# Optimization experiments

Hardware: AMD Instinct MI355X
Metric: run time of the kernel (lower is better)

The kernel has to match this reference:

```python
import jax, jax.numpy as jnp
import numpy as np

B, S, H, D = 4, 2048, 8, 64  # batch, seq, heads, per-head dim (dim=64)
EPS = 1e-5


def _layernorm(h, g, b):
    m = jnp.mean(h, axis=-1, keepdims=True)
    v = jnp.mean(jnp.square(h - m), axis=-1, keepdims=True)
    return (h - m) * jax.lax.rsqrt(v + EPS) * g + b


def setup_inputs() -> dict:
    key = jax.random.key(0)
    ks = jax.random.split(key, 12)
    s = 1.0 / np.sqrt(D)
    return {
        "x": jax.random.normal(ks[0], (B, S, H, D), dtype=jnp.float32),
        "ln1_g": jnp.ones((D,), jnp.float32),
        "ln1_b": jnp.zeros((D,), jnp.float32),
        "Wp": jax.random.normal(ks[1], (D, 3 * D), jnp.float32) * s,
        "bp": jnp.zeros((3 * D,), jnp.float32),
        "ln2_g": jnp.ones((D,), jnp.float32),
        "ln2_b": jnp.zeros((D,), jnp.float32),
        "W1": jax.random.normal(ks[2], (D, 4 * D), jnp.float32) * s,
        "b1": jnp.zeros((4 * D,), jnp.float32),
        "W2": jax.random.normal(ks[3], (4 * D, D), jnp.float32) * (1.0 / np.sqrt(4 * D)),
        "b2": jnp.zeros((D,), jnp.float32),
    }


def reference(x, ln1_g, ln1_b, Wp, bp, ln2_g, ln2_b, W1, b1, W2, b2):
    # x: [B, S, H, D]
    h = _layernorm(x, ln1_g, ln1_b)
    qkv = h @ Wp + bp                       # [B,S,H,3D]  (dropout = identity, eval)
    q, k, v = jnp.split(qkv, 3, axis=-1)
    q = q.transpose(0, 2, 1, 3)             # [B,H,S,D]
    k = k.transpose(0, 2, 1, 3)
    v = v.transpose(0, 2, 1, 3)
    sim = jnp.einsum('bhqd,bhkd->bhqk', q, k)   # no sqrt(d) scaling (faithful)
    attn = jax.nn.softmax(sim, axis=-1)
    out = jnp.einsum('bhqk,bhkd->bhqd', attn, v).transpose(0, 2, 1, 3)  # [B,S,H,D]
    out = _layernorm(out, ln2_g, ln2_b)
    out = jax.nn.gelu(out @ W1 + b1, approximate=False) @ W2 + b2
    return out + x
```

## Files before the change

kernel.cpp:

```cpp
#include <hip/hip_runtime.h>
#include <hip/hip_bf16.h>
#include <math.h>

#define BB 4
#define SS 2048
#define HH 8
#define DD 64
#define EPSV 1e-5f

typedef __attribute__((ext_vector_type(8))) short short8;
typedef __attribute__((ext_vector_type(4))) float f32x4;
typedef __attribute__((ext_vector_type(4))) unsigned int uint4v;
typedef unsigned short ushort_t;
#define MFMA16 __builtin_amdgcn_mfma_f32_16x16x32_bf16

__device__ inline unsigned short f2bf(float f) {
    unsigned u = __builtin_bit_cast(unsigned, f);
    unsigned r = (u + 0x7fffu + ((u >> 16) & 1u)) >> 16;
    return (unsigned short)r;
}
__device__ inline float bf2f(unsigned short h) {
    unsigned u = ((unsigned)h) << 16;
    return __builtin_bit_cast(float, u);
}
__device__ inline unsigned pkbf(float a, float b) {
    __hip_bfloat162 h2 = __float22bfloat162_rn(make_float2(a, b));
    unsigned u;
    __builtin_memcpy(&u, &h2, 4);
    return u;
}
__device__ inline float gelu_f(float v) {
    float a = v * 0.70710678118654752f;
    float z = fabsf(a);
    float t = __builtin_amdgcn_rcpf(fmaf(0.3275911f, z, 1.0f));
    float p = t * fmaf(t, fmaf(t, fmaf(t, fmaf(t, 1.061405429f, -1.453152027f),
                                       1.421413741f), -0.284496736f), 0.254829592f);
    float e = __builtin_amdgcn_exp2f(-z * z * 1.4426950408889634f);
    float erfz = fmaf(-p, e, 1.0f);
    float se = (a < 0.0f) ? -erfz : erfz;
    return 0.5f * v * (1.0f + se);
}

__global__ __launch_bounds__(256, 2) void k1_ln_qkv(
    const float* __restrict__ x, const float* __restrict__ g1, const float* __restrict__ b1v,
    const float* __restrict__ Wp, const float* __restrict__ bp,
    float* __restrict__ qws, ushort_t* __restrict__ khws, ushort_t* __restrict__ vtws)
{
    __shared__ __align__(16) ushort_t Hh[64 * 72];
    __shared__ __align__(16) ushort_t Hl[64 * 72];
    __shared__ __align__(16) ushort_t Vt[64 * 72];
    __shared__ __align__(16) ushort_t PadK1[13824];

    const int tid = threadIdx.x;
    const int wv  = tid >> 6;
    const int lane = tid & 63;
    const int l15 = lane & 15;
    const int g   = lane >> 4;
    const int bh  = blockIdx.x & 31;
    const int sc  = blockIdx.x >> 5;
    const int b   = bh >> 3, hh = bh & 7;
    const int s0  = sc * 64;

    PadK1[tid] = (ushort_t)tid;
    if (blockIdx.x == 0xFFFFFFFFu) {
        qws[tid] = (float)PadK1[255 - tid];
        return;
    }

    short8 bqh[2], bql[2], bkh[2], bkl[2], bvh[2];
    {
        const int nq = wv * 16 + l15;
        #pragma unroll
        for (int kh = 0; kh < 2; ++kh) {
            const int koff = kh * 32 + g * 8;
            #pragma unroll
            for (int j = 0; j < 8; ++j) {
                const float* wrow = Wp + (size_t)(koff + j) * 192 + nq;
                float wq = wrow[0];
                ushort_t hq = f2bf(wq);
                bqh[kh][j] = (short)hq;
                bql[kh][j] = (short)f2bf(wq - bf2f(hq));
                float wk = wrow[64];
                ushort_t hk = f2bf(wk);
                bkh[kh][j] = (short)hk;
                bkl[kh][j] = (short)f2bf(wk - bf2f(hk));
                bvh[kh][j] = (short)f2bf(wrow[128]);
            }
        }
    }
    const float biasq = bp[wv * 16 + l15];
    const float biask = bp[64 + wv * 16 + l15];
    const float biasv = bp[128 + wv * 16 + l15];

    {
        const int srow = s0 + wv * 16 + l15;
        const float* xr = x + ((size_t)(b * 2048 + srow) * 8 + hh) * 64;
        float hvv[16];
        #pragma unroll
        for (int kh = 0; kh < 2; ++kh) {
            float4 p0 = *(const float4*)(xr + kh * 32 + g * 8);
            float4 p1 = *(const float4*)(xr + kh * 32 + g * 8 + 4);
            hvv[kh*8+0]=p0.x; hvv[kh*8+1]=p0.y; hvv[kh*8+2]=p0.z; hvv[kh*8+3]=p0.w;
            hvv[kh*8+4]=p1.x; hvv[kh*8+5]=p1.y; hvv[kh*8+6]=p1.z; hvv[kh*8+7]=p1.w;
        }
        float s1 = 0.0f;
        #pragma unroll
        for (int i = 0; i < 16; ++i) s1 += hvv[i];
        s1 += __shfl_xor(s1, 16, 64);
        s1 += __shfl_xor(s1, 32, 64);
        float mean = s1 * (1.0f / 64.0f);
        float s2 = 0.0f;
        #pragma unroll
        for (int i = 0; i < 16; ++i) { float d = hvv[i] - mean; s2 += d * d; }
        s2 += __shfl_xor(s2, 16, 64);
        s2 += __shfl_xor(s2, 32, 64);
        float rstd = rsqrtf(s2 * (1.0f / 64.0f) + EPSV);

        #pragma unroll
        for (int kh = 0; kh < 2; ++kh) {
            ushort_t hi[8]; unsigned lo2[4];
            float hf[8];
            #pragma unroll
            for (int j = 0; j < 8; ++j) {
                int dI = kh * 32 + g * 8 + j;
                hf[j] = (hvv[kh*8+j] - mean) * rstd * g1[dI] + b1v[dI];
                hi[j] = f2bf(hf[j]);
            }
            uint4 HHv;
            HHv.x = (unsigned)hi[0] | ((unsigned)hi[1] << 16);
            HHv.y = (unsigned)hi[2] | ((unsigned)hi[3] << 16);
            HHv.z = (unsigned)hi[4] | ((unsigned)hi[5] << 16);
            HHv.w = (unsigned)hi[6] | ((unsigned)hi[7] << 16);
            #pragma unroll
            for (int j = 0; j < 4; ++j)
                lo2[j] = pkbf(hf[2*j] - bf2f(hi[2*j]), hf[2*j+1] - bf2f(hi[2*j+1]));
            uint4 HLv; HLv.x = lo2[0]; HLv.y = lo2[1]; HLv.z = lo2[2]; HLv.w = lo2[3];
            int off = (wv * 16 + l15) * 72 + kh * 32 + g * 8;
            *(uint4*)(&Hh[off]) = HHv;
            *(uint4*)(&Hl[off]) = HLv;
        }
    }
    __syncthreads();

    #pragma unroll
    for (int mt = 0; mt < 4; ++mt) {
        short8 ah[2], al[2];
        int abase = (mt * 16 + l15) * 72 + g * 8;
        ah[0] = *(const short8*)(&Hh[abase]);
        ah[1] = *(const short8*)(&Hh[abase + 32]);
        al[0] = *(const short8*)(&Hl[abase]);
        al[1] = *(const short8*)(&Hl[abase + 32]);

        f32x4 aq = (f32x4){0.f,0.f,0.f,0.f};
        f32x4 ak = (f32x4){0.f,0.f,0.f,0.f};
        f32x4 av = (f32x4){0.f,0.f,0.f,0.f};
        #pragma unroll
        for (int kh = 0; kh < 2; ++kh) {
            aq = MFMA16(ah[kh], bqh[kh], aq, 0, 0, 0);
            aq = MFMA16(al[kh], bqh[kh], aq, 0, 0, 0);
            aq = MFMA16(ah[kh], bql[kh], aq, 0, 0, 0);
            ak = MFMA16(ah[kh], bkh[kh], ak, 0, 0, 0);
            ak = MFMA16(al[kh], bkh[kh], ak, 0, 0, 0);
            ak = MFMA16(ah[kh], bkl[kh], ak, 0, 0, 0);
            av = MFMA16(ah[kh], bvh[kh], av, 0, 0, 0);
        }

        size_t base = ((size_t)bh * 2048 + s0 + mt * 16 + 4 * g) * 64 + wv * 16 + l15;
        #pragma unroll
        for (int r = 0; r < 4; ++r) {
            qws[base + (size_t)r * 64] = aq[r] + biasq;
            khws[base + (size_t)r * 64] = f2bf(ak[r] + biask);
        }
        uint2 vvp;
        vvp.x = pkbf(av[0] + biasv, av[1] + biasv);
        vvp.y = pkbf(av[2] + biasv, av[3] + biasv);
        *(uint2*)(&Vt[(wv * 16 + l15) * 72 + mt * 16 + 4 * g]) = vvp;
    }
    __syncthreads();

    #pragma unroll
    for (int p = 0; p < 2; ++p) {
        int slot = tid + 256 * p;
        int dd = slot >> 3, cc = slot & 7;
        int c0 = ((cc >> 2) << 5) + ((cc & 3) << 2);
        uint2 a = *(const uint2*)(&Vt[dd * 72 + c0]);
        uint2 b2 = *(const uint2*)(&Vt[dd * 72 + c0 + 16]);
        uint4 o; o.x = a.x; o.y = a.y; o.z = b2.x; o.w = b2.y;
        *(uint4*)(vtws + ((size_t)bh * 64 + dd) * 2048 + s0 + cc * 8) = o;
    }
}

#define NKT 32

__global__ __launch_bounds__(256, 2) void k2_attn(
    const float* __restrict__ qws, const ushort_t* __restrict__ khws,
    const ushort_t* __restrict__ vtws, float* __restrict__ ows)
{
    __shared__ __align__(16) ushort_t KhL[2][64 * 64];
    __shared__ __align__(16) ushort_t VtL[2][64 * 64];
    __shared__ __align__(16) ushort_t PadL[11264];

    const int tid  = threadIdx.x;
    const int w    = tid >> 6;
    const int lane = tid & 63;
    const int l15  = lane & 15;
    const int g    = lane >> 4;
    const int bh   = blockIdx.x & 31;
    const int qb0  = (blockIdx.x >> 5) * 128;

    PadL[tid] = (ushort_t)tid;
    if (blockIdx.x == 0xFFFFFFFFu) {
        ows[tid] = (float)PadL[255 - tid];
        return;
    }

    const float LOG2E = 1.4426950408889634f;
    short8 qh[2][2], ql[2][2];
    #pragma unroll
    for (int sub = 0; sub < 2; ++sub) {
        const float* qp = qws + ((size_t)bh * SS + qb0 + w * 32 + sub * 16 + l15) * 64;
        #pragma unroll
        for (int kh = 0; kh < 2; ++kh) {
            const float* p = qp + 32 * kh + 8 * g;
            #pragma unroll
            for (int j = 0; j < 8; ++j) {
                float f = p[j] * LOG2E;
                ushort_t hi = f2bf(f);
                qh[sub][kh][j] = (short)hi;
                ql[sub][kh][j] = (short)f2bf(f - bf2f(hi));
            }
        }
    }

    float lrow[2] = {0.0f, 0.0f};
    f32x4 oacc[2][4];
    #pragma unroll
    for (int sub = 0; sub < 2; ++sub)
        #pragma unroll
        for (int dt = 0; dt < 4; ++dt) oacc[sub][dt] = (f32x4){0.f, 0.f, 0.f, 0.f};

    const size_t kbase = (size_t)bh * SS * 64;
    const size_t vbase = (size_t)bh * 64 * 2048;

    const int dlo  = lane >> 3;
    const int j8   = ((lane & 7) ^ dlo) << 3;
    const int row0 = w * 8 + dlo;
    const int row1 = 32 + row0;
    const int lb0  = (64 * w) * 8;
    const int lb1  = (256 + 64 * w) * 8;

    #define K2_STAGE(buf, tg)                                                   \
        do {                                                                     \
            __builtin_amdgcn_global_load_lds(                                    \
                (const __attribute__((address_space(1))) void*)                  \
                    (khws + kbase + (size_t)((tg) * 64 + row0) * 64 + j8),       \
                (__attribute__((address_space(3))) void*)(&KhL[(buf)][lb0]),     \
                16, 0, 0);                                                       \
            __builtin_amdgcn_global_load_lds(                                    \
                (const __attribute__((address_space(1))) void*)                  \
                    (khws + kbase + (size_t)((tg) * 64 + row1) * 64 + j8),       \
                (__attribute__((address_space(3))) void*)(&KhL[(buf)][lb1]),     \
                16, 0, 0);                                                       \
            __builtin_amdgcn_global_load_lds(                                    \
                (const __attribute__((address_space(1))) void*)                  \
                    (vtws + vbase + (size_t)row0 * 2048 + (tg) * 64 + j8),       \
                (__attribute__((address_space(3))) void*)(&VtL[(buf)][lb0]),     \
                16, 0, 0);                                                       \
            __builtin_amdgcn_global_load_lds(                                    \
                (const __attribute__((address_space(1))) void*)                  \
                    (vtws + vbase + (size_t)row1 * 2048 + (tg) * 64 + j8),       \
                (__attribute__((address_space(3))) void*)(&VtL[(buf)][lb1]),     \
                16, 0, 0);                                                       \
        } while (0)

    K2_STAGE(0, 0);

    const int rsw = l15 & 7;

    for (int kt = 0; kt < NKT; ++kt) {
        __syncthreads();
        const int cur = kt & 1;

        if (kt < NKT - 1) K2_STAGE(cur ^ 1, kt + 1);

        #pragma unroll
        for (int half = 0; half < 2; ++half) {
            uint2 pA[2], pB[2];
            #pragma unroll
            for (int nf2 = 0; nf2 < 2; ++nf2) {
                const int nf = half * 2 + nf2;
                f32x4 aA = (f32x4){0.f, 0.f, 0.f, 0.f};
                f32x4 aB = (f32x4){0.f, 0.f, 0.f, 0.f};
                #pragma unroll
                for (int kh = 0; kh < 2; ++kh) {
                    short8 kah = *(const short8*)(
                        &KhL[cur][(nf * 16 + l15) * 64 + (((4 * kh + g) ^ rsw) << 3)]);
                    aA = MFMA16(kah, qh[0][kh], aA, 0, 0, 0);
                    aA = MFMA16(kah, ql[0][kh], aA, 0, 0, 0);
                    aB = MFMA16(kah, qh[1][kh], aB, 0, 0, 0);
                    aB = MFMA16(kah, ql[1][kh], aB, 0, 0, 0);
                }
                {
                    float p0 = __builtin_amdgcn_exp2f(aA[0]);
                    float p1 = __builtin_amdgcn_exp2f(aA[1]);
                    float p2 = __builtin_amdgcn_exp2f(aA[2]);
                    float p3 = __builtin_amdgcn_exp2f(aA[3]);
                    lrow[0] += (p0 + p1) + (p2 + p3);
                    pA[nf2].x = pkbf(p0, p1); pA[nf2].y = pkbf(p2, p3);
                }
                {
                    float p0 = __builtin_amdgcn_exp2f(aB[0]);
                    float p1 = __builtin_amdgcn_exp2f(aB[1]);
                    float p2 = __builtin_amdgcn_exp2f(aB[2]);
                    float p3 = __builtin_amdgcn_exp2f(aB[3]);
                    lrow[1] += (p0 + p1) + (p2 + p3);
                    pB[nf2].x = pkbf(p0, p1); pB[nf2].y = pkbf(p2, p3);
                }
            }
            short8 paA = __builtin_bit_cast(short8, (uint4v){pA[0].x, pA[0].y, pA[1].x, pA[1].y});
            short8 paB = __builtin_bit_cast(short8, (uint4v){pB[0].x, pB[0].y, pB[1].x, pB[1].y});
            #pragma unroll
            for (int dt = 0; dt < 4; ++dt) {
                short8 vbf = *(const short8*)(
                    &VtL[cur][(16 * dt + l15) * 64 + (((4 * half + g) ^ rsw) << 3)]);
                oacc[0][dt] = MFMA16(paA, vbf, oacc[0][dt], 0, 0, 0);
                oacc[1][dt] = MFMA16(paB, vbf, oacc[1][dt], 0, 0, 0);
            }
        }
    }

    #pragma unroll
    for (int sub = 0; sub < 2; ++sub) {
        float l = lrow[sub];
        l += __shfl_xor(l, 16, 64);
        l += __shfl_xor(l, 32, 64);
        float il = 1.0f / l;
        #pragma unroll
        for (int r = 0; r < 4; ++r) {
            float ilr = __shfl(il, 4 * g + r, 64);
            int row = qb0 + w * 32 + sub * 16 + 4 * g + r;
            #pragma unroll
            for (int dt = 0; dt < 4; ++dt)
                ows[((size_t)bh * SS + row) * 64 + dt * 16 + l15] = oacc[sub][dt][r] * ilr;
        }
    }
    #undef K2_STAGE
}

__global__ __launch_bounds__(256, 2) void k3_ln_mlp(
    const float* __restrict__ ows, const float* __restrict__ x,
    const float* __restrict__ g2, const float* __restrict__ b2v,
    const float* __restrict__ W1, const float* __restrict__ b1m,
    const float* __restrict__ W2, const float* __restrict__ b2o,
    float* __restrict__ out)
{
    __shared__ __align__(16) ushort_t Hb[64 * 72];
    __shared__ __align__(16) ushort_t Hs[16 * 264];
    __shared__ __align__(16) float Rs[4 * 16 * 72];
    __shared__ __align__(16) ushort_t PadK3[9600];

    const int tid  = threadIdx.x;
    const int wv   = tid >> 6;
    const int lane = tid & 63;
    const int l15  = lane & 15;
    const int g    = lane >> 4;

    PadK3[tid] = (ushort_t)tid;
    if (blockIdx.x == 0xFFFFFFFFu) {
        out[tid] = (float)PadK3[255 - tid];
        return;
    }

    short8 w1f[4][2], w2f[4][2];
    float  b1r[4][4];
    #pragma unroll
    for (int t = 0; t < 4; ++t) {
        #pragma unroll
        for (int kh = 0; kh < 2; ++kh) {
            #pragma unroll
            for (int j = 0; j < 8; ++j) {
                w1f[t][kh][j] = (short)f2bf(
                    W1[(size_t)(kh * 32 + g * 8 + j) * 256 + wv * 64 + t * 16 + l15]);
                w2f[t][kh][j] = (short)f2bf(
                    W2[(size_t)(wv * 64 + kh * 32 + g * 8 + j) * 64 + t * 16 + l15]);
            }
        }
        #pragma unroll
        for (int r = 0; r < 4; ++r)
            b1r[t][r] = b1m[wv * 64 + t * 16 + 4 * g + r];
    }

    const int r0 = blockIdx.x * 64;

    {
        const float* orow = ows + (size_t)(r0 + wv * 16 + l15) * 64;
        float hvv[16];
        #pragma unroll
        for (int kh = 0; kh < 2; ++kh) {
            float4 p0 = *(const float4*)(orow + kh * 32 + g * 8);
            float4 p1 = *(const float4*)(orow + kh * 32 + g * 8 + 4);
            hvv[kh*8+0]=p0.x; hvv[kh*8+1]=p0.y; hvv[kh*8+2]=p0.z; hvv[kh*8+3]=p0.w;
            hvv[kh*8+4]=p1.x; hvv[kh*8+5]=p1.y; hvv[kh*8+6]=p1.z; hvv[kh*8+7]=p1.w;
        }
        float s1 = 0.0f;
        #pragma unroll
        for (int i = 0; i < 16; ++i) s1 += hvv[i];
        s1 += __shfl_xor(s1, 16, 64);
        s1 += __shfl_xor(s1, 32, 64);
        float mean = s1 * (1.0f / 64.0f);
        float s2 = 0.0f;
        #pragma unroll
        for (int i = 0; i < 16; ++i) { float d = hvv[i] - mean; s2 += d * d; }
        s2 += __shfl_xor(s2, 16, 64);
        s2 += __shfl_xor(s2, 32, 64);
        float rstd = rsqrtf(s2 * (1.0f / 64.0f) + EPSV);

        #pragma unroll
        for (int kh = 0; kh < 2; ++kh) {
            ushort_t hi[8];
            #pragma unroll
            for (int j = 0; j < 8; ++j) {
                int dI = kh * 32 + g * 8 + j;
                hi[j] = f2bf((hvv[kh*8+j] - mean) * rstd * g2[dI] + b2v[dI]);
            }
            uint4 HHv;
            HHv.x = (unsigned)hi[0] | ((unsigned)hi[1] << 16);
            HHv.y = (unsigned)hi[2] | ((unsigned)hi[3] << 16);
            HHv.z = (unsigned)hi[4] | ((unsigned)hi[5] << 16);
            HHv.w = (unsigned)hi[6] | ((unsigned)hi[7] << 16);
            *(uint4*)(&Hb[(wv * 16 + l15) * 72 + kh * 32 + g * 8]) = HHv;
        }
    }
    __syncthreads();

    for (int mt = 0; mt < 4; ++mt) {
        short8 h2f[2];
        h2f[0] = *(const short8*)(&Hb[(mt * 16 + l15) * 72 + g * 8]);
        h2f[1] = *(const short8*)(&Hb[(mt * 16 + l15) * 72 + 32 + g * 8]);

        #pragma unroll
        for (int t = 0; t < 4; ++t) {
            f32x4 acc = (f32x4){0.f, 0.f, 0.f, 0.f};
            acc = MFMA16(w1f[t][0], h2f[0], acc, 0, 0, 0);
            acc = MFMA16(w1f[t][1], h2f[1], acc, 0, 0, 0);
            float ge[4];
            #pragma unroll
            for (int r = 0; r < 4; ++r)
                ge[r] = gelu_f(acc[r] + b1r[t][r]);
            uint2 pk;
            pk.x = pkbf(ge[0], ge[1]);
            pk.y = pkbf(ge[2], ge[3]);
            *(uint2*)(&Hs[l15 * 264 + wv * 64 + t * 16 + 4 * g]) = pk;
        }

        short8 ha[2];
        ha[0] = *(const short8*)(&Hs[l15 * 264 + wv * 64 + g * 8]);
        ha[1] = *(const short8*)(&Hs[l15 * 264 + wv * 64 + 32 + g * 8]);
        #pragma unroll
        for (int t = 0; t < 4; ++t) {
            f32x4 a2 = (f32x4){0.f, 0.f, 0.f, 0.f};
            a2 = MFMA16(ha[0], w2f[t][0], a2, 0, 0, 0);
            a2 = MFMA16(ha[1], w2f[t][1], a2, 0, 0, 0);
            #pragma unroll
            for (int r = 0; r < 4; ++r)
                Rs[wv * 1152 + (4 * g + r) * 72 + t * 16 + l15] = a2[r];
        }
        __syncthreads();

        {
            int m = tid >> 4, d4 = tid & 15;
            const float* rp = Rs + m * 72 + d4 * 4;
            f32x4 v0 = *(const f32x4*)(rp);
            f32x4 v1 = *(const f32x4*)(rp + 1152);
            f32x4 v2 = *(const f32x4*)(rp + 2304);
            f32x4 v3 = *(const f32x4*)(rp + 3456);
            f32x4 sum = v0 + v1 + v2 + v3;
            int r = r0 + mt * 16 + m;
            int bq = r >> 14, hq = (r >> 11) & 7, sq = r & 2047;
            size_t oidx = ((size_t)(bq * 2048 + sq) * 8 + hq) * 64 + d4 * 4;
            float4 xv = *(const float4*)(x + oidx);
            float4 bo = *(const float4*)(b2o + d4 * 4);
            float4 res = make_float4(sum[0] + xv.x + bo.x, sum[1] + xv.y + bo.y,
                                     sum[2] + xv.z + bo.z, sum[3] + xv.w + bo.w);
            *(float4*)(out + oidx) = res;
        }
        __syncthreads();
    }
}

extern "C" void kernel_launch(void* const* d_in, const int* in_sizes, int n_in,
                              void* d_out, int out_size, void* d_ws, size_t ws_size,
                              hipStream_t stream) {
    const float* x     = (const float*)d_in[0];
    const float* ln1_g = (const float*)d_in[1];
    const float* ln1_b = (const float*)d_in[2];
    const float* Wp    = (const float*)d_in[3];
    const float* bp    = (const float*)d_in[4];
    const float* ln2_g = (const float*)d_in[5];
    const float* ln2_b = (const float*)d_in[6];
    const float* W1    = (const float*)d_in[7];
    const float* b1    = (const float*)d_in[8];
    const float* W2    = (const float*)d_in[9];
    const float* b2    = (const float*)d_in[10];
    float* out = (float*)d_out;

    float* ws  = (float*)d_ws;
    float* qws = ws;
    float* ows = ws + 4194304;
    ushort_t* khws = (ushort_t*)(ws + 8388608);
    ushort_t* vtws = khws + 4194304;

    k1_ln_qkv<<<dim3(1024), dim3(256), 0, stream>>>(
        x, ln1_g, ln1_b, Wp, bp, qws, khws, vtws);
    k2_attn<<<dim3(512), dim3(256), 0, stream>>>(qws, khws, vtws, ows);
    k3_ln_mlp<<<dim3(1024), dim3(256), 0, stream>>>(
        ows, x, ln2_g, ln2_b, W1, b1, W2, b2, out);
}
```

Before: 168.5 us.

## Split attention KV range across two half-blocks and merge partial outputs

The attention kernel now launches 512 threads per block, with two groups of four waves each processing half of the key/value sequence for the same 128 query rows. Partial outputs and row sums from the second half are combined through shared memory at the end. K/V staging changes from asynchronous global-to-LDS loads with an XOR swizzle to register prefetch plus padded LDS rows. This doubles per-block parallelism and cuts the serial K loop length, at the cost of an extra barrier per tile, a final reduction step, and the loss of the async copy path.

Measured after the change: 212.8 us. +26.3%, slower.

```diff
diff --git a/kernel.cpp b/kernel.cpp
--- a/kernel.cpp
+++ b/kernel.cpp
@@ -190,27 +190,30 @@
     }
 }
 
-#define NKT 32
-
-__global__ __launch_bounds__(256, 2) void k2_attn(
+#define LROW 72
+#define NKTH 16
+
+__global__ __launch_bounds__(512, 2) void k2_attn(
     const float* __restrict__ qws, const ushort_t* __restrict__ khws,
     const ushort_t* __restrict__ vtws, float* __restrict__ ows)
 {
-    __shared__ __align__(16) ushort_t KhL[2][64 * 64];
-    __shared__ __align__(16) ushort_t VtL[2][64 * 64];
-    __shared__ __align__(16) ushort_t PadL[11264];
+    __shared__ __align__(16) ushort_t SM[2][2][64 * LROW];
+    __shared__ __align__(16) ushort_t PadL[9216];
 
     const int tid  = threadIdx.x;
     const int w    = tid >> 6;
+    const int hw   = w >> 2;
+    const int w4   = w & 3;
     const int lane = tid & 63;
     const int l15  = lane & 15;
     const int g    = lane >> 4;
+    const int tid4 = tid & 255;
     const int bh   = blockIdx.x & 31;
     const int qb0  = (blockIdx.x >> 5) * 128;
 
     PadL[tid] = (ushort_t)tid;
     if (blockIdx.x == 0xFFFFFFFFu) {
-        ows[tid] = (float)PadL[255 - tid];
+        ows[tid] = (float)PadL[511 - tid];
         return;
     }
 
@@ -218,7 +221,7 @@
     short8 qh[2][2], ql[2][2];
     #pragma unroll
     for (int sub = 0; sub < 2; ++sub) {
-        const float* qp = qws + ((size_t)bh * SS + qb0 + w * 32 + sub * 16 + l15) * 64;
+        const float* qp = qws + ((size_t)bh * SS + qb0 + w4 * 32 + sub * 16 + l15) * 64;
         #pragma unroll
         for (int kh = 0; kh < 2; ++kh) {
             const float* p = qp + 32 * kh + 8 * g;
@@ -242,46 +245,35 @@
     const size_t kbase = (size_t)bh * SS * 64;
     const size_t vbase = (size_t)bh * 64 * 2048;
 
-    const int dlo  = lane >> 3;
-    const int j8   = ((lane & 7) ^ dlo) << 3;
-    const int row0 = w * 8 + dlo;
-    const int row1 = 32 + row0;
-    const int lb0  = (64 * w) * 8;
-    const int lb1  = (256 + 64 * w) * 8;
-
-    #define K2_STAGE(buf, tg)                                                   \
-        do {                                                                     \
-            __builtin_amdgcn_global_load_lds(                                    \
-                (const __attribute__((address_space(1))) void*)                  \
-                    (khws + kbase + (size_t)((tg) * 64 + row0) * 64 + j8),       \
-                (__attribute__((address_space(3))) void*)(&KhL[(buf)][lb0]),     \
-                16, 0, 0);                                                       \
-            __builtin_amdgcn_global_load_lds(                                    \
-                (const __attribute__((address_space(1))) void*)                  \
-                    (khws + kbase + (size_t)((tg) * 64 + row1) * 64 + j8),       \
-                (__attribute__((address_space(3))) void*)(&KhL[(buf)][lb1]),     \
-                16, 0, 0);                                                       \
-            __builtin_amdgcn_global_load_lds(                                    \
-                (const __attribute__((address_space(1))) void*)                  \
-                    (vtws + vbase + (size_t)row0 * 2048 + (tg) * 64 + j8),       \
-                (__attribute__((address_space(3))) void*)(&VtL[(buf)][lb0]),     \
-                16, 0, 0);                                                       \
-            __builtin_amdgcn_global_load_lds(                                    \
-                (const __attribute__((address_space(1))) void*)                  \
-                    (vtws + vbase + (size_t)row1 * 2048 + (tg) * 64 + j8),       \
-                (__attribute__((address_space(3))) void*)(&VtL[(buf)][lb1]),     \
-                16, 0, 0);                                                       \
-        } while (0)
-
-    K2_STAGE(0, 0);
-
-    const int rsw = l15 & 7;
-
-    for (int kt = 0; kt < NKT; ++kt) {
+    const int row0 = (tid4) >> 3,        seg0 = tid4 & 7;
+    const int row1 = (tid4 + 256) >> 3,  seg1 = (tid4 + 256) & 7;
+
+    uint4 kb[2], vb[2];
+    {
+        int tg = hw * NKTH;
+        kb[0] = *(const uint4*)(khws + kbase + (size_t)(tg * 64 + row0) * 64 + seg0 * 8);
+        vb[0] = *(const uint4*)(vtws + vbase + (size_t)row0 * 2048 + tg * 64 + seg0 * 8);
+        kb[1] = *(const uint4*)(khws + kbase + (size_t)(tg * 64 + row1) * 64 + seg1 * 8);
+        vb[1] = *(const uint4*)(vtws + vbase + (size_t)row1 * 2048 + tg * 64 + seg1 * 8);
+    }
+
+    for (int kt = 0; kt < NKTH; ++kt) {
         __syncthreads();
-        const int cur = kt & 1;
-
-        if (kt < NKT - 1) K2_STAGE(cur ^ 1, kt + 1);
+        *(uint4*)(&SM[hw][0][row0 * LROW + seg0 * 8]) = kb[0];
+        *(uint4*)(&SM[hw][1][row0 * LROW + seg0 * 8]) = vb[0];
+        *(uint4*)(&SM[hw][0][row1 * LROW + seg1 * 8]) = kb[1];
+        *(uint4*)(&SM[hw][1][row1 * LROW + seg1 * 8]) = vb[1];
+        __syncthreads();
+        const ushort_t* KhL = &SM[hw][0][0];
+        const ushort_t* VtL = &SM[hw][1][0];
+
+        if (kt < NKTH - 1) {
+            int tg = hw * NKTH + kt + 1;
+            kb[0] = *(const uint4*)(khws + kbase + (size_t)(tg * 64 + row0) * 64 + seg0 * 8);
+            vb[0] = *(const uint4*)(vtws + vbase + (size_t)row0 * 2048 + tg * 64 + seg0 * 8);
+            kb[1] = *(const uint4*)(khws + kbase + (size_t)(tg * 64 + row1) * 64 + seg1 * 8);
+            vb[1] = *(const uint4*)(vtws + vbase + (size_t)row1 * 2048 + tg * 64 + seg1 * 8);
+        }
 
         #pragma unroll
         for (int half = 0; half < 2; ++half) {
@@ -293,8 +285,7 @@
                 f32x4 aB = (f32x4){0.f, 0.f, 0.f, 0.f};
                 #pragma unroll
                 for (int kh = 0; kh < 2; ++kh) {
-                    short8 kah = *(const short8*)(
-                        &KhL[cur][(nf * 16 + l15) * 64 + (((4 * kh + g) ^ rsw) << 3)]);
+                    short8 kah = *(const short8*)(&KhL[(nf * 16 + l15) * LROW + 32 * kh + 8 * g]);
                     aA = MFMA16(kah, qh[0][kh], aA, 0, 0, 0);
                     aA = MFMA16(kah, ql[0][kh], aA, 0, 0, 0);
                     aB = MFMA16(kah, qh[1][kh], aB, 0, 0, 0);
@@ -321,12 +312,34 @@
             short8 paB = __builtin_bit_cast(short8, (uint4v){pB[0].x, pB[0].y, pB[1].x, pB[1].y});
             #pragma unroll
             for (int dt = 0; dt < 4; ++dt) {
-                short8 vbf = *(const short8*)(
-                    &VtL[cur][(16 * dt + l15) * 64 + (((4 * half + g) ^ rsw) << 3)]);
+                short8 vbf = *(const short8*)(&VtL[(16 * dt + l15) * LROW + half * 32 + 8 * g]);
                 oacc[0][dt] = MFMA16(paA, vbf, oacc[0][dt], 0, 0, 0);
                 oacc[1][dt] = MFMA16(paB, vbf, oacc[1][dt], 0, 0, 0);
             }
         }
+    }
+
+    __syncthreads();
+    float* cmb = (float*)&SM[0][0][0];
+    float* rec = cmb + (w4 * 64 + lane) * 36;
+    if (hw == 1) {
+        #pragma unroll
+        for (int sub = 0; sub < 2; ++sub) {
+            #pragma unroll
+            for (int dt = 0; dt < 4; ++dt)
+                *(f32x4*)(rec + sub * 16 + dt * 4) = oacc[sub][dt];
+            rec[32 + sub] = lrow[sub];
+        }
+    }
+    __syncthreads();
+    if (hw == 1) return;
+
+    #pragma unroll
+    for (int sub = 0; sub < 2; ++sub) {
+        #pragma unroll
+        for (int dt = 0; dt < 4; ++dt)
+            oacc[sub][dt] += *(const f32x4*)(rec + sub * 16 + dt * 4);
+        lrow[sub] += rec[32 + sub];
     }
 
     #pragma unroll
@@ -338,13 +351,12 @@
         #pragma unroll
         for (int r = 0; r < 4; ++r) {
             float ilr = __shfl(il, 4 * g + r, 64);
-            int row = qb0 + w * 32 + sub * 16 + 4 * g + r;
+            int row = qb0 + w4 * 32 + sub * 16 + 4 * g + r;
             #pragma unroll
             for (int dt = 0; dt < 4; ++dt)
                 ows[((size_t)bh * SS + row) * 64 + dt * 16 + l15] = oacc[sub][dt][r] * ilr;
         }
     }
-    #undef K2_STAGE
 }
 
 __global__ __launch_bounds__(256, 2) void k3_ln_mlp(
@@ -512,7 +524,7 @@
 
     k1_ln_qkv<<<dim3(1024), dim3(256), 0, stream>>>(
         x, ln1_g, ln1_b, Wp, bp, qws, khws, vtws);
-    k2_attn<<<dim3(512), dim3(256), 0, stream>>>(qws, khws, vtws, ows);
+    k2_attn<<<dim3(512), dim3(512), 0, stream>>>(qws, khws, vtws, ows);
     k3_ln_mlp<<<dim3(1024), dim3(256), 0, stream>>>(
         ows, x, ln2_g, ln2_b, W1, b1, W2, b2, out);
 }
```
